# Kernel tuning notes

Hardware: AMD Instinct MI355X
Metric: run time of the kernel (lower is better)

The kernel has to match this reference:

```python
import jax, jax.numpy as jnp
import numpy as np

CODE_LEN = 1024
INFO_LEN = 512
BATCH = 2048
ITERS = 5
CLIP = 15.0
N_STAGES = 10  # log2(CODE_LEN)
DESIGN_SNR = 0.0


def _bhattacharyya_info_idx(N, K, snr_db):
    # standard polar code construction: Bhattacharyya parameter recursion
    z = np.array([np.exp(-10.0 ** (snr_db / 10.0))], dtype=np.float64)
    while z.size < N:
        z = np.concatenate([2.0 * z - z ** 2, z ** 2])
    return np.sort(np.argsort(z)[:K]).astype(np.int32)


def setup_inputs() -> dict:
    key = jax.random.key(0)
    rx = jax.random.normal(key, (BATCH, CODE_LEN), dtype=jnp.float32) * 4.0  # channel LLRs
    info_idx = jnp.asarray(_bhattacharyya_info_idx(CODE_LEN, INFO_LEN, DESIGN_SNR))
    return {"rx": rx, "info_idx": info_idx}


def _split(x, s):
    # pair elements (i, i + 2^s) within blocks of size 2^(s+1)
    B, N = x.shape
    st = 1 << s
    xr = x.reshape(B, N // (2 * st), 2, st)
    return xr[:, :, 0, :], xr[:, :, 1, :]


def _merge(u, l, s):
    B = u.shape[0]
    return jnp.stack([u, l], axis=2).reshape(B, -1)


def _f(a, b):
    # min-sum check-node update
    return jnp.sign(a) * jnp.sign(b) * jnp.minimum(jnp.abs(a), jnp.abs(b))


def _clip(x):
    return jnp.clip(x, -CLIP, CLIP)


def _iterate_right(right, left):
    # sweep info side (stage 0) -> channel side (stage n)
    cur = right[:, 0]
    stages = [cur]
    for s in range(N_STAGES):
        r_u, r_l = _split(cur, s)
        l_u, l_l = _split(left[:, s + 1], s)
        n_u = _clip(_f(r_u, l_l + r_l))
        n_l = _clip(_f(r_u, l_u) + r_l)
        cur = _merge(n_u, n_l, s)
        stages.append(cur)
    return jnp.stack(stages, axis=1)


def _iterate_left(right, left):
    # sweep channel side (stage n) -> info side (stage 0)
    cur = left[:, N_STAGES]
    stages = [cur]
    for s in range(N_STAGES - 1, -1, -1):
        l_u, l_l = _split(cur, s)
        r_u, r_l = _split(right[:, s], s)
        n_u = _clip(_f(l_u, l_l + r_l))
        n_l = _clip(_f(r_u, l_u) + l_l)
        cur = _merge(n_u, n_l, s)
        stages.append(cur)
    return jnp.stack(stages[::-1], axis=1)


def reference(rx, info_idx):
    B = rx.shape[0]
    mask = jnp.zeros((CODE_LEN,), rx.dtype).at[info_idx].set(1.0)
    # frozen positions carry +clip LLR, info positions 0 (crc=[], so total_info_bits == info mask)
    right = jnp.zeros((B, N_STAGES + 1, CODE_LEN), rx.dtype).at[:, 0].set((1.0 - mask) * CLIP)
    left = jnp.zeros_like(right).at[:, N_STAGES].set(rx)
    u_list = []
    for _ in range(ITERS):  # filter_in_iterations_eval=False -> all rows active every iteration
        right = _iterate_right(right, left)
        left = _iterate_left(right, left)
        u = left[:, 0] + right[:, 0]
        u_list.append(jnp.take(u, info_idx, axis=1))
    u_list.append(u_list[-1])  # u_list[-1] scatter reduces to last iterate when all rows active
    return jnp.stack(u_list)  # [ITERS+1, B, INFO_LEN]
```

## Files before the change

### kernel.cpp

```cpp
#include <hip/hip_runtime.h>

constexpr int CODE_LEN = 1024;
constexpr int INFO_LEN = 512;
constexpr int BATCH    = 2048;
constexpr int ITERS    = 5;
#define CLIPV 15.0f

__device__ __forceinline__ float fop(float a, float b) {
    float m = fminf(fabsf(a), fabsf(b));
    unsigned s = (__float_as_uint(a) ^ __float_as_uint(b)) & 0x80000000u;
    return __uint_as_float(__float_as_uint(m) | s);
}
__device__ __forceinline__ float clipf(float x) {
    return __builtin_amdgcn_fmed3f(x, -CLIPV, CLIPV);
}


#define RSTEP0(A, B) do { \
    float bu0=(B)[0], bl0=(B)[1], bu1=(B)[2], bl1=(B)[3]; \
    (B)[0]=clipf(fop((A)[0], bl0+(A)[1])); \
    (B)[1]=clipf(fop((A)[0], bu0)+(A)[1]); \
    (B)[2]=clipf(fop((A)[2], bl1+(A)[3])); \
    (B)[3]=clipf(fop((A)[2], bu1)+(A)[3]); } while(0)
#define RSTEP1(A, B) do { \
    float bu0=(B)[0], bl0=(B)[2], bu1=(B)[1], bl1=(B)[3]; \
    (B)[0]=clipf(fop((A)[0], bl0+(A)[2])); \
    (B)[2]=clipf(fop((A)[0], bu0)+(A)[2]); \
    (B)[1]=clipf(fop((A)[1], bl1+(A)[3])); \
    (B)[3]=clipf(fop((A)[1], bu1)+(A)[3]); } while(0)
#define LSTEP0(A, B) do { \
    float au0=(A)[0], al0=(A)[1], au1=(A)[2], al1=(A)[3]; \
    (A)[0]=clipf(fop((B)[0], (B)[1]+al0)); \
    (A)[1]=clipf(fop(au0, (B)[0])+(B)[1]); \
    (A)[2]=clipf(fop((B)[2], (B)[3]+al1)); \
    (A)[3]=clipf(fop(au1, (B)[2])+(B)[3]); } while(0)
#define LSTEP1(A, B) do { \
    float au0=(A)[0], al0=(A)[2], au1=(A)[1], al1=(A)[3]; \
    (A)[0]=clipf(fop((B)[0], (B)[2]+al0)); \
    (A)[2]=clipf(fop(au0, (B)[0])+(B)[2]); \
    (A)[1]=clipf(fop((B)[1], (B)[3]+al1)); \
    (A)[3]=clipf(fop(au1, (B)[1])+(B)[3]); } while(0)

#define CONV_W(arr, BETA) do { \
    float* wb_ = &WB[(t >> 6) * 256]; \
    const int l6_ = t & 63; \
    *(float4*)&wb_[l6_ * 4] = make_float4((arr)[0], (arr)[1], (arr)[2], (arr)[3]); \
    const int rb_ = ((l6_ & ~(3 << (BETA))) << 2) | ((l6_ >> (BETA)) & 3); \
    (arr)[0] = wb_[rb_]; \
    (arr)[1] = wb_[rb_ + (4  << (BETA))]; \
    (arr)[2] = wb_[rb_ + (8  << (BETA))]; \
    (arr)[3] = wb_[rb_ + (12 << (BETA))]; } while(0)

#define CONV_X(arr, XBUF) do { \
    *(float4*)&(XBUF)[t * 4] = make_float4((arr)[0], (arr)[1], (arr)[2], (arr)[3]); \
    __syncthreads(); \
    const int rb_ = (t & 63) * 4 + (t >> 6); \
    (arr)[0] = (XBUF)[rb_]; \
    (arr)[1] = (XBUF)[rb_ + 256]; \
    (arr)[2] = (XBUF)[rb_ + 512]; \
    (arr)[3] = (XBUF)[rb_ + 768]; } while(0)

__global__ __launch_bounds__(256, 4) void polar_bp_r7(const float* __restrict__ rx,
                                                      const int* __restrict__ info,
                                                      float* __restrict__ out) {
    __shared__ int   RK[CODE_LEN];
    __shared__ float WB[CODE_LEN];
    __shared__ float XB0[CODE_LEN];
    __shared__ float XB1[CODE_LEN];

    const int t = threadIdx.x;
    const int b = blockIdx.x;

    *(int4*)&RK[t * 4] = make_int4(-1, -1, -1, -1);
    __syncthreads();
#pragma unroll
    for (int k = 0; k < 2; ++k) {
        int kk = t + 256 * k;
        int p  = info[kk];
        int fl = (p & 3) | (((p >> 6) & 3) << 2) | (((p >> 4) & 3) << 4)
               | (((p >> 2) & 3) << 6) | (((p >> 8) & 3) << 8);
        RK[fl] = kk;
    }
    __syncthreads();

    float S[10][4];
    {
        const float* rxb = rx + (size_t)b * CODE_LEN
                         + ((t >> 6) & 3) * 64 + (t & 3) * 16
                         + ((t >> 2) & 3) * 4 + ((t >> 4) & 3);
        S[9][0] = rxb[0];   S[9][1] = rxb[256];
        S[9][2] = rxb[512]; S[9][3] = rxb[768];
    }
#pragma unroll
    for (int s = 0; s < 9; ++s)
#pragma unroll
        for (int j = 0; j < 4; ++j) S[s][j] = 0.f;

#pragma unroll 1
    for (int it = 0; it < ITERS; ++it) {
        {
            int4 rkv = *(const int4*)&RK[t * 4];
            float fr[4];
            fr[0] = rkv.x < 0 ? CLIPV : 0.f;  fr[1] = rkv.y < 0 ? CLIPV : 0.f;
            fr[2] = rkv.z < 0 ? CLIPV : 0.f;  fr[3] = rkv.w < 0 ? CLIPV : 0.f;
            RSTEP0(fr, S[0]);
        }
        RSTEP1(S[0], S[1]);
        CONV_W(S[1], 4);
        RSTEP0(S[1], S[2]);
        RSTEP1(S[2], S[3]);
        CONV_W(S[3], 2);
        RSTEP0(S[3], S[4]);
        RSTEP1(S[4], S[5]);
        CONV_W(S[5], 0);
        RSTEP0(S[5], S[6]);
        RSTEP1(S[6], S[7]);
        CONV_X(S[7], XB0);
        RSTEP0(S[7], S[8]);
        LSTEP1(S[8], S[9]);
        LSTEP0(S[7], S[8]);
        CONV_X(S[7], XB1);
        LSTEP1(S[6], S[7]);
        LSTEP0(S[5], S[6]);
        CONV_W(S[5], 0);
        LSTEP1(S[4], S[5]);
        LSTEP0(S[3], S[4]);
        CONV_W(S[3], 2);
        LSTEP1(S[2], S[3]);
        LSTEP0(S[1], S[2]);
        CONV_W(S[1], 4);
        LSTEP1(S[0], S[1]);
        {
            int4 rkv = *(const int4*)&RK[t * 4];
            float f0 = rkv.x < 0 ? CLIPV : 0.f, f1 = rkv.y < 0 ? CLIPV : 0.f;
            float f2 = rkv.z < 0 ? CLIPV : 0.f, f3 = rkv.w < 0 ? CLIPV : 0.f;
            float v0 = clipf(fop(S[0][0], S[0][1] + f1));
            float v1 = clipf(fop(f0, S[0][0]) + S[0][1]);
            float v2 = clipf(fop(S[0][2], S[0][3] + f3));
            float v3 = clipf(fop(f2, S[0][2]) + S[0][3]);
            float* ob = out + ((size_t)it * BATCH + b) * INFO_LEN;
            if (rkv.x >= 0) ob[rkv.x] = v0;
            if (rkv.y >= 0) ob[rkv.y] = v1;
            if (rkv.z >= 0) ob[rkv.z] = v2;
            if (rkv.w >= 0) ob[rkv.w] = v3;
            if (it == ITERS - 1) {
                float* ob2 = ob + (size_t)BATCH * INFO_LEN;
                if (rkv.x >= 0) ob2[rkv.x] = v0;
                if (rkv.y >= 0) ob2[rkv.y] = v1;
                if (rkv.z >= 0) ob2[rkv.z] = v2;
                if (rkv.w >= 0) ob2[rkv.w] = v3;
            }
        }
    }
}

extern "C" void kernel_launch(void* const* d_in, const int* in_sizes, int n_in,
                              void* d_out, int out_size, void* d_ws, size_t ws_size,
                              hipStream_t stream) {
    const float* rx   = (const float*)d_in[0];
    const int*   info = (const int*)d_in[1];
    float*       outp = (float*)d_out;
    polar_bp_r7<<<dim3(BATCH), dim3(256), 0, stream>>>(rx, info, outp);
}
```

Before: 39.15 us.

## Drop redundant clips, swizzle LDS transposes, hoist frozen mask and output indexing

Removes the clip on min-sum outputs whose inputs are already bounded: the min of two clipped magnitudes cannot exceed the clip. A full-clip variant is kept only where the raw channel LLRs enter. The warp-local LDS transposes now use an XOR-swizzled layout with precomputed read offsets, to avoid bank conflicts and per-call index arithmetic. The frozen-mask load, its select logic and the output pointer math move out of the iteration loop, and the duplicated last-iteration store becomes a single write after the loop. This cuts ALU work and LDS conflicts per stage, at the cost of slightly more live registers.

```diff
diff --git a/kernel.cpp b/kernel.cpp
--- a/kernel.cpp
+++ b/kernel.cpp
@@ -18,49 +18,47 @@
 
 #define RSTEP0(A, B) do { \
     float bu0=(B)[0], bl0=(B)[1], bu1=(B)[2], bl1=(B)[3]; \
-    (B)[0]=clipf(fop((A)[0], bl0+(A)[1])); \
+    (B)[0]=fop((A)[0], bl0+(A)[1]); \
     (B)[1]=clipf(fop((A)[0], bu0)+(A)[1]); \
-    (B)[2]=clipf(fop((A)[2], bl1+(A)[3])); \
+    (B)[2]=fop((A)[2], bl1+(A)[3]); \
     (B)[3]=clipf(fop((A)[2], bu1)+(A)[3]); } while(0)
 #define RSTEP1(A, B) do { \
     float bu0=(B)[0], bl0=(B)[2], bu1=(B)[1], bl1=(B)[3]; \
-    (B)[0]=clipf(fop((A)[0], bl0+(A)[2])); \
+    (B)[0]=fop((A)[0], bl0+(A)[2]); \
     (B)[2]=clipf(fop((A)[0], bu0)+(A)[2]); \
-    (B)[1]=clipf(fop((A)[1], bl1+(A)[3])); \
+    (B)[1]=fop((A)[1], bl1+(A)[3]); \
     (B)[3]=clipf(fop((A)[1], bu1)+(A)[3]); } while(0)
 #define LSTEP0(A, B) do { \
     float au0=(A)[0], al0=(A)[1], au1=(A)[2], al1=(A)[3]; \
-    (A)[0]=clipf(fop((B)[0], (B)[1]+al0)); \
+    (A)[0]=fop((B)[0], (B)[1]+al0); \
     (A)[1]=clipf(fop(au0, (B)[0])+(B)[1]); \
-    (A)[2]=clipf(fop((B)[2], (B)[3]+al1)); \
+    (A)[2]=fop((B)[2], (B)[3]+al1); \
     (A)[3]=clipf(fop(au1, (B)[2])+(B)[3]); } while(0)
 #define LSTEP1(A, B) do { \
+    float au0=(A)[0], al0=(A)[2], au1=(A)[1], al1=(A)[3]; \
+    (A)[0]=fop((B)[0], (B)[2]+al0); \
+    (A)[2]=clipf(fop(au0, (B)[0])+(B)[2]); \
+    (A)[1]=fop((B)[1], (B)[3]+al1); \
+    (A)[3]=clipf(fop(au1, (B)[1])+(B)[3]); } while(0)
+#define LSTEP1C(A, B) do { \
     float au0=(A)[0], al0=(A)[2], au1=(A)[1], al1=(A)[3]; \
     (A)[0]=clipf(fop((B)[0], (B)[2]+al0)); \
     (A)[2]=clipf(fop(au0, (B)[0])+(B)[2]); \
     (A)[1]=clipf(fop((B)[1], (B)[3]+al1)); \
     (A)[3]=clipf(fop(au1, (B)[1])+(B)[3]); } while(0)
 
-#define CONV_W(arr, BETA) do { \
-    float* wb_ = &WB[(t >> 6) * 256]; \
-    const int l6_ = t & 63; \
-    *(float4*)&wb_[l6_ * 4] = make_float4((arr)[0], (arr)[1], (arr)[2], (arr)[3]); \
-    const int rb_ = ((l6_ & ~(3 << (BETA))) << 2) | ((l6_ >> (BETA)) & 3); \
-    (arr)[0] = wb_[rb_]; \
-    (arr)[1] = wb_[rb_ + (4  << (BETA))]; \
-    (arr)[2] = wb_[rb_ + (8  << (BETA))]; \
-    (arr)[3] = wb_[rb_ + (12 << (BETA))]; } while(0)
+#define CONV_W(arr, R) do { \
+    *(float4*)&WB[offW] = make_float4((arr)[0], (arr)[1], (arr)[2], (arr)[3]); \
+    float c0_ = WB[(R)[0]], c1_ = WB[(R)[1]], c2_ = WB[(R)[2]], c3_ = WB[(R)[3]]; \
+    (arr)[0]=c0_; (arr)[1]=c1_; (arr)[2]=c2_; (arr)[3]=c3_; } while(0)
 
 #define CONV_X(arr, XBUF) do { \
-    *(float4*)&(XBUF)[t * 4] = make_float4((arr)[0], (arr)[1], (arr)[2], (arr)[3]); \
+    *(float4*)&(XBUF)[offXw] = make_float4((arr)[0], (arr)[1], (arr)[2], (arr)[3]); \
     __syncthreads(); \
-    const int rb_ = (t & 63) * 4 + (t >> 6); \
-    (arr)[0] = (XBUF)[rb_]; \
-    (arr)[1] = (XBUF)[rb_ + 256]; \
-    (arr)[2] = (XBUF)[rb_ + 512]; \
-    (arr)[3] = (XBUF)[rb_ + 768]; } while(0)
+    (arr)[0]=(XBUF)[offXr];     (arr)[1]=(XBUF)[offXr+256]; \
+    (arr)[2]=(XBUF)[offXr+512]; (arr)[3]=(XBUF)[offXr+768]; } while(0)
 
-__global__ __launch_bounds__(256, 4) void polar_bp_r7(const float* __restrict__ rx,
+__global__ __launch_bounds__(256, 4) void polar_bp_r8(const float* __restrict__ rx,
                                                       const int* __restrict__ info,
                                                       float* __restrict__ out) {
     __shared__ int   RK[CODE_LEN];
@@ -83,6 +81,27 @@
     }
     __syncthreads();
 
+    const int l6 = t & 63;
+    const int wbase = (t >> 6) * 256;
+    const int offW  = wbase + 4 * (l6 ^ (l6 >> 2));
+    int offR4[4], offR2[4], offR0[4];
+#pragma unroll
+    for (int k = 0; k < 4; ++k) {
+        int g4 = (l6 & ~(3 << 4)) | (k << 4);
+        int g2 = (l6 & ~(3 << 2)) | (k << 2);
+        int g0 = (l6 & ~3) | k;
+        offR4[k] = wbase + 4 * (g4 ^ (g4 >> 2)) + ((l6 >> 4) & 3);
+        offR2[k] = wbase + 4 * (g2 ^ (g2 >> 2)) + ((l6 >> 2) & 3);
+        offR0[k] = wbase + 4 * (g0 ^ (g0 >> 2)) + (l6 & 3);
+    }
+    const int offXw = t * 4;
+    const int offXr = (t & 63) * 4 + (t >> 6);
+
+    const int4 rkv = *(const int4*)&RK[t * 4];
+    float fr[4];
+    fr[0] = rkv.x < 0 ? CLIPV : 0.f;  fr[1] = rkv.y < 0 ? CLIPV : 0.f;
+    fr[2] = rkv.z < 0 ? CLIPV : 0.f;  fr[3] = rkv.w < 0 ? CLIPV : 0.f;
+
     float S[10][4];
     {
         const float* rxb = rx + (size_t)b * CODE_LEN
@@ -96,62 +115,52 @@
 #pragma unroll
         for (int j = 0; j < 4; ++j) S[s][j] = 0.f;
 
+    float v0, v1, v2, v3;
+    float* ob = out + (size_t)b * INFO_LEN;
+    const size_t obstride = (size_t)BATCH * INFO_LEN;
+
 #pragma unroll 1
     for (int it = 0; it < ITERS; ++it) {
-        {
-            int4 rkv = *(const int4*)&RK[t * 4];
-            float fr[4];
-            fr[0] = rkv.x < 0 ? CLIPV : 0.f;  fr[1] = rkv.y < 0 ? CLIPV : 0.f;
-            fr[2] = rkv.z < 0 ? CLIPV : 0.f;  fr[3] = rkv.w < 0 ? CLIPV : 0.f;
-            RSTEP0(fr, S[0]);
-        }
+        RSTEP0(fr, S[0]);
         RSTEP1(S[0], S[1]);
-        CONV_W(S[1], 4);
+        CONV_W(S[1], offR4);
         RSTEP0(S[1], S[2]);
         RSTEP1(S[2], S[3]);
-        CONV_W(S[3], 2);
+        CONV_W(S[3], offR2);
         RSTEP0(S[3], S[4]);
         RSTEP1(S[4], S[5]);
-        CONV_W(S[5], 0);
+        CONV_W(S[5], offR0);
         RSTEP0(S[5], S[6]);
         RSTEP1(S[6], S[7]);
         CONV_X(S[7], XB0);
         RSTEP0(S[7], S[8]);
-        LSTEP1(S[8], S[9]);
+        LSTEP1C(S[8], S[9]);
         LSTEP0(S[7], S[8]);
         CONV_X(S[7], XB1);
         LSTEP1(S[6], S[7]);
         LSTEP0(S[5], S[6]);
-        CONV_W(S[5], 0);
+        CONV_W(S[5], offR0);
         LSTEP1(S[4], S[5]);
         LSTEP0(S[3], S[4]);
-        CONV_W(S[3], 2);
+        CONV_W(S[3], offR2);
         LSTEP1(S[2], S[3]);
         LSTEP0(S[1], S[2]);
-        CONV_W(S[1], 4);
+        CONV_W(S[1], offR4);
         LSTEP1(S[0], S[1]);
-        {
-            int4 rkv = *(const int4*)&RK[t * 4];
-            float f0 = rkv.x < 0 ? CLIPV : 0.f, f1 = rkv.y < 0 ? CLIPV : 0.f;
-            float f2 = rkv.z < 0 ? CLIPV : 0.f, f3 = rkv.w < 0 ? CLIPV : 0.f;
-            float v0 = clipf(fop(S[0][0], S[0][1] + f1));
-            float v1 = clipf(fop(f0, S[0][0]) + S[0][1]);
-            float v2 = clipf(fop(S[0][2], S[0][3] + f3));
-            float v3 = clipf(fop(f2, S[0][2]) + S[0][3]);
-            float* ob = out + ((size_t)it * BATCH + b) * INFO_LEN;
-            if (rkv.x >= 0) ob[rkv.x] = v0;
-            if (rkv.y >= 0) ob[rkv.y] = v1;
-            if (rkv.z >= 0) ob[rkv.z] = v2;
-            if (rkv.w >= 0) ob[rkv.w] = v3;
-            if (it == ITERS - 1) {
-                float* ob2 = ob + (size_t)BATCH * INFO_LEN;
-                if (rkv.x >= 0) ob2[rkv.x] = v0;
-                if (rkv.y >= 0) ob2[rkv.y] = v1;
-                if (rkv.z >= 0) ob2[rkv.z] = v2;
-                if (rkv.w >= 0) ob2[rkv.w] = v3;
-            }
-        }
+        v0 = fop(S[0][0], S[0][1] + fr[1]);
+        v1 = clipf(fop(fr[0], S[0][0]) + S[0][1]);
+        v2 = fop(S[0][2], S[0][3] + fr[3]);
+        v3 = clipf(fop(fr[2], S[0][2]) + S[0][3]);
+        if (rkv.x >= 0) ob[rkv.x] = v0;
+        if (rkv.y >= 0) ob[rkv.y] = v1;
+        if (rkv.z >= 0) ob[rkv.z] = v2;
+        if (rkv.w >= 0) ob[rkv.w] = v3;
+        ob += obstride;
     }
+    if (rkv.x >= 0) ob[rkv.x] = v0;
+    if (rkv.y >= 0) ob[rkv.y] = v1;
+    if (rkv.z >= 0) ob[rkv.z] = v2;
+    if (rkv.w >= 0) ob[rkv.w] = v3;
 }
 
 extern "C" void kernel_launch(void* const* d_in, const int* in_sizes, int n_in,
@@ -160,5 +169,5 @@
     const float* rx   = (const float*)d_in[0];
     const int*   info = (const int*)d_in[1];
     float*       outp = (float*)d_out;
-    polar_bp_r7<<<dim3(BATCH), dim3(256), 0, stream>>>(rx, info, outp);
+    polar_bp_r8<<<dim3(BATCH), dim3(256), 0, stream>>>(rx, info, outp);
 }
```

Result: no change. 38.40 us (-1.9%).
